# Kernel tuning notes

Measured on AMD Instinct MI355X. Metric: run time of the kernel, lower is better.

Reference implementation:

```python
import jax, jax.numpy as jnp
import numpy as np
import math

B, L, C, D, H, NLAYERS, DFF = 256, 100, 55, 512, 8, 3, 64


def _pos_embedding(length, d_model):
    pos = np.arange(length, dtype=np.float32)[:, None]
    div = np.exp(np.arange(0, d_model, 2, dtype=np.float32) * (-math.log(10000.0) / d_model))
    pe = np.zeros((length, d_model), dtype=np.float32)
    pe[:, 0::2] = np.sin(pos * div)
    pe[:, 1::2] = np.cos(pos * div)
    return jnp.asarray(pe)


def setup_inputs() -> dict:
    key = jax.random.key(0)
    ks = jax.random.split(key, 12)
    r = lambda k, s, sc: jax.random.normal(k, s, dtype=jnp.float32) * sc
    sD = 1.0 / math.sqrt(D)
    return {
        'x': r(ks[0], (B, L, C), 1.0),
        'tok_w': r(ks[1], (D, C, 3), 1.0 / math.sqrt(3 * C)),  # Conv1d(c_in->d_model, k=3, circular, no bias)
        'pe': _pos_embedding(L, D),
        'Wq': r(ks[2], (NLAYERS, D, D), sD), 'bq': jnp.zeros((NLAYERS, D), jnp.float32),
        'Wk': r(ks[3], (NLAYERS, D, D), sD), 'bk': jnp.zeros((NLAYERS, D), jnp.float32),
        'Wv': r(ks[4], (NLAYERS, D, D), sD), 'bv': jnp.zeros((NLAYERS, D), jnp.float32),
        'Wsig': r(ks[5], (NLAYERS, H, D), sD), 'bsig': jnp.zeros((NLAYERS, H), jnp.float32),
        'Wo': r(ks[6], (NLAYERS, D, D), sD), 'bo': jnp.zeros((NLAYERS, D), jnp.float32),
        'W1': r(ks[7], (NLAYERS, DFF, D), sD), 'b1': jnp.zeros((NLAYERS, DFF), jnp.float32),  # conv1 (1x1)
        'W2': r(ks[8], (NLAYERS, D, DFF), 1.0 / math.sqrt(DFF)), 'b2': jnp.zeros((NLAYERS, D), jnp.float32),  # conv2 (1x1)
        'proj_w': r(ks[9], (C, D), sD), 'proj_b': jnp.zeros((C,), jnp.float32),
    }


def _forward(x, tok_w, pe, Wq, bq, Wk, bk, Wv, bv, Wsig, bsig, Wo, bo, W1, b1, W2, b2, proj_w, proj_b):
    Bx, Lx, _ = x.shape
    nlayers, nH = Wsig.shape[0], Wsig.shape[1]
    d_model = Wq.shape[1]
    dk = d_model // nH
    scale = 1.0 / math.sqrt(dk)
    # token embedding: circular-padded Conv1d(k=3, no bias), then + positional embedding
    xc = jnp.pad(jnp.swapaxes(x, 1, 2), ((0, 0), (0, 0), (1, 1)), mode='wrap')  # [B,C,L+2]
    emb = jax.lax.conv_general_dilated(xc, tok_w, (1,), 'VALID', dimension_numbers=('NCW', 'OIW', 'NCW'))
    h = jnp.swapaxes(emb, 1, 2) + pe[None]  # [B,L,D]
    dist = jnp.abs(jnp.arange(Lx)[:, None] - jnp.arange(Lx)[None, :]).astype(h.dtype)  # |i-j|
    for l in range(nlayers):
        q = h @ Wq[l].T + bq[l]                       # [B,L,D]
        k = (h @ Wk[l].T + bk[l]).reshape(Bx, Lx, nH, dk)
        v = (h @ Wv[l].T + bv[l]).reshape(Bx, Lx, nH, dk)
        # NOTE: source applies sigma projection to the *projected* queries
        sigma = q @ Wsig[l].T + bsig[l]               # [B,L,H]
        qh = q.reshape(Bx, Lx, nH, dk)
        scores = jnp.einsum('blhe,bshe->bhls', qh, k)  # [B,H,L,L]
        series = jax.nn.softmax(scale * scores, axis=-1)
        # Gaussian prior branch (mask_flag=False; computed in source forward,
        # does not feed the module's returned output)
        sg = jnp.swapaxes(sigma, 1, 2)                 # [B,H,L]
        sg = jnp.power(3.0, jax.nn.sigmoid(sg * 5.0) + 1e-5) - 1.0
        sgE = sg[..., None]                            # [B,H,L,1]
        _prior = jnp.exp(-(dist ** 2)[None, None] / (2.0 * sgE ** 2)) / (math.sqrt(2.0 * math.pi) * sgE)
        o = jnp.einsum('bhls,bshd->blhd', series, v).reshape(Bx, Lx, d_model)
        h = h + (o @ Wo[l].T + bo[l])                  # residual 1 (dropout=identity at eval)
        y = jax.nn.gelu(h @ W1[l].T + b1[l], approximate=False)  # conv1 1x1 + gelu
        h = h + (y @ W2[l].T + b2[l])                  # conv2 1x1, residual 2
    return h @ proj_w.T + proj_b                       # [B,L,c_out]


def reference(x, tok_w, pe, Wq, bq, Wk, bk, Wv, bv, Wsig, bsig, Wo, bo, W1, b1, W2, b2, proj_w, proj_b):
    return _forward(x, tok_w, pe, Wq, bq, Wk, bk, Wv, bv, Wsig, bsig, Wo, bo, W1, b1, W2, b2, proj_w, proj_b)
```

## Files before the change

### kernel.cpp

```cpp
#include <hip/hip_runtime.h>
#include <stdint.h>

typedef unsigned short u16;
typedef __attribute__((ext_vector_type(8))) short short8;
typedef __attribute__((ext_vector_type(4))) float f32x4;

#define DEVI __device__ __forceinline__

#define BB   256
#define LL   100
#define CC   55
#define DD   512
#define HH   8
#define DKK  64
#define MM   (BB * LL)
#define KEMB 192
#define NSEG 17

DEVI float bf2f(u16 s) { union { unsigned int u; float f; } x; x.u = ((unsigned int)s) << 16; return x.f; }
DEVI u16 f2bf(float f) {
  union { float f; unsigned int u; } x; x.f = f;
  unsigned int u = x.u;
  return (u16)((u + 0x7FFFu + ((u >> 16) & 1u)) >> 16);
}

DEVI void async_lds16(const u16* gp, u16* lp) {
  __builtin_amdgcn_global_load_lds((const __attribute__((address_space(1))) void*)gp,
                                   (__attribute__((address_space(3))) void*)lp, 16, 0, 0);
}

DEVI void wave_lds_fence() {
  asm volatile("s_waitcnt lgkmcnt(0)" ::: "memory");
  __builtin_amdgcn_wave_barrier();
}

DEVI int swz_row(int r) { return (r & 3) ^ ((r >> 2) & 3); }

__global__ void detect_dtype(const u16* __restrict__ x, int* __restrict__ flag) {
  __shared__ int cnt[256];
  int tid = threadIdx.x;
  u16 u = x[2 * tid];
  int e = (u >> 7) & 0xFF;
  cnt[tid] = (e >= 0x5F && e <= 0x90) ? 1 : 0;
  __syncthreads();
  for (int s = 128; s > 0; s >>= 1) { if (tid < s) cnt[tid] += cnt[tid + s]; __syncthreads(); }
  if (tid == 0) *flag = (cnt[0] >= 160) ? 0 : 1;
}

struct Segs { const void* src[NSEG]; int off[NSEG + 1]; };

__global__ void convert_all(Segs s, const int* __restrict__ flag, u16* __restrict__ dst) {
  int i = blockIdx.x * 256 + threadIdx.x;
  if (i >= s.off[NSEG]) return;
  int sidx = 0;
#pragma unroll
  for (int k = 1; k < NSEG; k++) if (i >= s.off[k]) sidx = k;
  int j = i - s.off[sidx];
  u16 v;
  if (*flag) v = f2bf(((const float*)s.src[sidx])[j]);
  else       v = ((const u16*)s.src[sidx])[j];
  dst[i] = v;
}

__global__ void repack_w(const u16* __restrict__ tokw, u16* __restrict__ Wg) {
  int idx = blockIdx.x * 256 + threadIdx.x;
  if (idx >= 512 * KEMB) return;
  int d = idx / KEMB, j = idx % KEMB, k = j >> 6, c = j & 63;
  Wg[idx] = (c < CC) ? tokw[d * (CC * 3) + c * 3 + k] : (u16)0;
}

__global__ void repack_x(const u16* __restrict__ x, u16* __restrict__ Xg) {
  int idx = blockIdx.x * 256 + threadIdx.x;
  if (idx >= MM * KEMB) return;
  int m = idx / KEMB, j = idx % KEMB, k = j >> 6, c = j & 63;
  int b = m / LL, l = m % LL;
  int l2 = l + k - 1; l2 = (l2 + LL) % LL;
  Xg[idx] = (c < CC) ? x[(size_t)(b * LL + l2) * CC + c] : (u16)0;
}

struct GemmW { const u16* W[3]; const u16* bias[3]; void* out[3]; };

template<int BM, int BN, int NTT, int TAG, bool QKV, bool DIRECT>
__global__ __launch_bounds__(256)
void gemm_bt(const u16* __restrict__ A, int K, GemmW w,
             const u16* __restrict__ pe,
             const u16* __restrict__ resid,
             int dogelu,
             int ldo, int nvalid,
             const int* __restrict__ dtf)
{
  constexpr int BK = 32;
  constexpr int MI = BM / 32;
  constexpr int CW = BN / 2, NT = CW / 16;
  constexpr int SW = CW + 4;
  constexpr int S_BUF = (BM + BN) * BK;
  __shared__ alignas(16) u16 smem[2 * S_BUF];

  const int tid = threadIdx.x;
  const int lane = tid & 63;
  const int wv = __builtin_amdgcn_readfirstlane(tid >> 6);
  const int wm = wv & 1, wn = wv >> 1;
  const int l15 = lane & 15, qd = lane >> 4;
  const int swz = swz_row(l15);

  const int id = blockIdx.x;
  const int mpx = gridDim.x / (NTT * 8);
  const int xcd = id & 7, slot = id >> 3;
  const int m_t = xcd * mpx + slot / NTT;
  const int n_t = slot % NTT;
  const int m0 = m_t * BM;
  int n0 = n_t * BN;
  int sel = 0, n0l = n0;
  if (QKV) { sel = n0 >> 9; n0l = n0 & 511; }
  const u16* W = w.W[sel];
  const u16* bias = w.bias[sel];
  void* outp = w.out[sel];

  const f32x4 zf = {0.f, 0.f, 0.f, 0.f};
  f32x4 acc[MI][NT];
#pragma unroll
  for (int i = 0; i < MI; i++)
#pragma unroll
    for (int j = 0; j < NT; j++) acc[i][j] = zf;

  auto STAGE = [&](int buf, int kp) {
    u16* Asp = smem + buf * S_BUF;
    u16* Bsp = Asp + BM * BK;
#pragma unroll
    for (int i = 0; i < BM / 64; i++) {
      int base = i * 256 + wv * 64;
      int idx = base + lane;
      int row = idx >> 2;
      int cs = ((idx & 3) ^ swz_row(row)) * 8;
      async_lds16(A + (size_t)(m0 + row) * K + kp + cs, Asp + base * 8);
    }
#pragma unroll
    for (int i = 0; i < BN / 64; i++) {
      int base = i * 256 + wv * 64;
      int idx = base + lane;
      int row = idx >> 2;
      int cs = ((idx & 3) ^ swz_row(row)) * 8;
      int gr = n0l + row; if (gr >= nvalid) gr = nvalid - 1;
      async_lds16(W + (size_t)gr * K + kp + cs, Bsp + base * 8);
    }
  };

  const int NBK = K >> 5;
  STAGE(0, 0);
  __syncthreads();
  int cur = 0;
  for (int ks = 0; ks < NBK; ks++) {
    if (ks + 1 < NBK) STAGE(cur ^ 1, (ks + 1) << 5);
    const u16* Asp = smem + cur * S_BUF;
    const u16* Bsp = Asp + BM * BK;
    short8 af[MI], bfr[NT];
#pragma unroll
    for (int mi = 0; mi < MI; mi++)
      af[mi] = *(const short8*)&Asp[(wm * (BM / 2) + mi * 16 + l15) * BK + ((qd ^ swz) * 8)];
#pragma unroll
    for (int ni = 0; ni < NT; ni++)
      bfr[ni] = *(const short8*)&Bsp[(wn * CW + ni * 16 + l15) * BK + ((qd ^ swz) * 8)];
#pragma unroll
    for (int mi = 0; mi < MI; mi++)
#pragma unroll
      for (int ni = 0; ni < NT; ni++)
        acc[mi][ni] = __builtin_amdgcn_mfma_f32_16x16x32_bf16(af[mi], bfr[ni], acc[mi][ni], 0, 0, 0);
    __syncthreads();
    cur ^= 1;
  }

  if (DIRECT) {
    const int sf = (dtf != nullptr) ? *dtf : 0;
#pragma unroll
    for (int mi = 0; mi < MI; mi++)
#pragma unroll
      for (int ni = 0; ni < NT; ni++) {
        int gcol = n0l + wn * CW + ni * 16 + l15;
        float bv = (bias && gcol < nvalid) ? bf2f(bias[gcol]) : 0.f;
#pragma unroll
        for (int r = 0; r < 4; r++) {
          int grow = m0 + wm * (BM / 2) + mi * 16 + qd * 4 + r;
          if (gcol < nvalid) {
            float v = acc[mi][ni][r] + bv;
            if (sf) ((float*)outp)[(size_t)grow * ldo + gcol] = v;
            else    ((u16*)outp)[(size_t)grow * ldo + gcol] = f2bf(v);
          }
        }
      }
    return;
  }

  u16* slab = smem + wv * 16 * SW;
#pragma unroll
  for (int mi = 0; mi < MI; mi++) {
    const int lr = wm * (BM / 2) + mi * 16 + qd * 4;
    float v[NT][4];
    if (!QKV && resid) {
#pragma unroll
      for (int ni = 0; ni < NT; ni++) {
        int col = n0l + wn * CW + ni * 16 + l15;
#pragma unroll
        for (int r = 0; r < 4; r++)
          v[ni][r] = bf2f(resid[(size_t)(m0 + lr + r) * DD + col]);
      }
    } else {
#pragma unroll
      for (int ni = 0; ni < NT; ni++)
#pragma unroll
        for (int r = 0; r < 4; r++) v[ni][r] = 0.f;
    }
#pragma unroll
    for (int ni = 0; ni < NT; ni++) {
      const int lc = wn * CW + ni * 16 + l15;
      float bv = bias ? bf2f(bias[n0l + lc]) : 0.f;
#pragma unroll
      for (int r = 0; r < 4; r++) {
        float x = v[ni][r] + acc[mi][ni][r] + bv;
        if (!QKV && pe) x += bf2f(pe[((m0 + lr + r) % LL) * DD + n0l + lc]);
        if (!QKV && dogelu) x = 0.5f * x * (1.f + erff(x * 0.70710678118654752f));
        v[ni][r] = x;
      }
    }
#pragma unroll
    for (int ni = 0; ni < NT; ni++)
#pragma unroll
      for (int r = 0; r < 4; r++)
        slab[(qd * 4 + r) * SW + ni * 16 + l15] = f2bf(v[ni][r]);
    wave_lds_fence();
    if (BN == 128) {
      int r2 = lane >> 2, c2 = (lane & 3) * 16;
      int grow = m0 + wm * (BM / 2) + mi * 16 + r2;
      u16* op = (u16*)outp + (size_t)grow * ldo + n0l + wn * CW + c2;
      *(short8*)&op[0] = *(const short8*)&slab[r2 * SW + c2];
      *(short8*)&op[8] = *(const short8*)&slab[r2 * SW + c2 + 8];
    } else {
      if (lane < 32) {
        int r2 = lane >> 1, c2 = (lane & 1) * 16;
        int grow = m0 + wm * (BM / 2) + mi * 16 + r2;
        u16* op = (u16*)outp + (size_t)grow * ldo + n0l + wn * CW + c2;
        *(short8*)&op[0] = *(const short8*)&slab[r2 * SW + c2];
        *(short8*)&op[8] = *(const short8*)&slab[r2 * SW + c2 + 8];
      }
    }
    wave_lds_fence();
  }
}

__global__ __launch_bounds__(256)
void ffn_fused(const u16* __restrict__ h, const u16* __restrict__ W1,
               const u16* __restrict__ b1, const u16* __restrict__ W2,
               const u16* __restrict__ b2, u16* __restrict__ hout)
{
  constexpr int BM = 64, BK = 32, SW = 36;
  __shared__ alignas(16) u16 smem[4096 + 10496];
  u16* y      = smem;
  u16* shared = smem + 4096;
  u16* As  = shared;
  u16* Bs  = shared + 4096;
  u16* Bs2 = shared;
  u16* slabs = shared + 8192;

  const int tid = threadIdx.x;
  const int lane = tid & 63;
  const int wv = __builtin_amdgcn_readfirstlane(tid >> 6);
  const int wm = wv & 1, wn = wv >> 1;
  const int l15 = lane & 15, qd = lane >> 4;
  const int swz = swz_row(l15);
  const int id = blockIdx.x;
  const int mpx = gridDim.x >> 3;
  const int m0 = ((id & 7) * mpx + (id >> 3)) * BM;

  const int srow = tid >> 2;
  const int scs = ((tid & 3) ^ swz_row(srow)) * 8;
  const f32x4 zf = {0.f, 0.f, 0.f, 0.f};

  f32x4 acc[2][2];
#pragma unroll
  for (int i = 0; i < 2; i++)
#pragma unroll
    for (int j = 0; j < 2; j++) acc[i][j] = zf;

  for (int k0 = 0; k0 < DD; k0 += 64) {
    __syncthreads();
#pragma unroll
    for (int p = 0; p < 2; p++) {
      const int kp = k0 + p * BK;
      async_lds16(h  + (size_t)(m0 + srow) * DD + kp + scs, As + p * 2048 + tid * 8);
      async_lds16(W1 + (size_t)srow * DD + kp + scs,        Bs + p * 2048 + tid * 8);
    }
    __syncthreads();
#pragma unroll
    for (int p = 0; p < 2; p++) {
      short8 af[2], bfr[2];
#pragma unroll
      for (int mi = 0; mi < 2; mi++)
        af[mi] = *(const short8*)&As[p * 2048 + (wm * 32 + mi * 16 + l15) * BK + ((qd ^ swz) * 8)];
#pragma unroll
      for (int ni = 0; ni < 2; ni++)
        bfr[ni] = *(const short8*)&Bs[p * 2048 + (wn * 32 + ni * 16 + l15) * BK + ((qd ^ swz) * 8)];
#pragma unroll
      for (int mi = 0; mi < 2; mi++)
#pragma unroll
        for (int ni = 0; ni < 2; ni++)
          acc[mi][ni] = __builtin_amdgcn_mfma_f32_16x16x32_bf16(af[mi], bfr[ni], acc[mi][ni], 0, 0, 0);
    }
  }
#pragma unroll
  for (int mi = 0; mi < 2; mi++)
#pragma unroll
    for (int ni = 0; ni < 2; ni++) {
      float bv = bf2f(b1[wn * 32 + ni * 16 + l15]);
#pragma unroll
      for (int r = 0; r < 4; r++) {
        int row = wm * 32 + mi * 16 + qd * 4 + r;
        int kpos = ni * 16 + l15;
        int slot = ((kpos >> 3) ^ swz_row(row)) & 3;
        float x = acc[mi][ni][r] + bv;
        x = 0.5f * x * (1.f + erff(x * 0.70710678118654752f));
        y[wn * 2048 + row * BK + slot * 8 + (kpos & 7)] = f2bf(x);
      }
    }
  __syncthreads();

  auto stage2 = [&](int buf, int nc) {
#pragma unroll
    for (int p = 0; p < 2; p++)
      async_lds16(W2 + (size_t)(nc * 64 + srow) * 64 + p * BK + scs,
                  Bs2 + buf * 4096 + p * 2048 + tid * 8);
  };
  stage2(0, 0);
  int cur = 0;
  u16* slab = slabs + wv * 16 * SW;
  for (int nc = 0; nc < 8; nc++) {
    __syncthreads();
    if (nc + 1 < 8) stage2(cur ^ 1, nc + 1);
    f32x4 a2[2][2];
#pragma unroll
    for (int i = 0; i < 2; i++)
#pragma unroll
      for (int j = 0; j < 2; j++) a2[i][j] = zf;
#pragma unroll
    for (int p = 0; p < 2; p++) {
      short8 af[2], bfr[2];
#pragma unroll
      for (int mi = 0; mi < 2; mi++)
        af[mi] = *(const short8*)&y[p * 2048 + (wm * 32 + mi * 16 + l15) * BK + ((qd ^ swz) * 8)];
#pragma unroll
      for (int ni = 0; ni < 2; ni++)
        bfr[ni] = *(const short8*)&Bs2[cur * 4096 + p * 2048 + (wn * 32 + ni * 16 + l15) * BK + ((qd ^ swz) * 8)];
#pragma unroll
      for (int mi = 0; mi < 2; mi++)
#pragma unroll
        for (int ni = 0; ni < 2; ni++)
          a2[mi][ni] = __builtin_amdgcn_mfma_f32_16x16x32_bf16(af[mi], bfr[ni], a2[mi][ni], 0, 0, 0);
    }
    const int n0l = nc * 64;
#pragma unroll
    for (int mi = 0; mi < 2; mi++) {
      const int lr = wm * 32 + mi * 16 + qd * 4;
      float v[2][4];
#pragma unroll
      for (int ni = 0; ni < 2; ni++) {
        int col = n0l + wn * 32 + ni * 16 + l15;
        float bv = bf2f(b2[col]);
#pragma unroll
        for (int r = 0; r < 4; r++)
          v[ni][r] = bf2f(h[(size_t)(m0 + lr + r) * DD + col]) + a2[mi][ni][r] + bv;
      }
#pragma unroll
      for (int ni = 0; ni < 2; ni++)
#pragma unroll
        for (int r = 0; r < 4; r++)
          slab[(qd * 4 + r) * SW + ni * 16 + l15] = f2bf(v[ni][r]);
      wave_lds_fence();
      if (lane < 32) {
        int r2 = lane >> 1, c2 = (lane & 1) * 16;
        int grow = m0 + wm * 32 + mi * 16 + r2;
        u16* op = hout + (size_t)grow * DD + n0l + wn * 32 + c2;
        *(short8*)&op[0] = *(const short8*)&slab[r2 * SW + c2];
        *(short8*)&op[8] = *(const short8*)&slab[r2 * SW + c2 + 8];
      }
      wave_lds_fence();
    }
    cur ^= 1;
  }
}

__global__ __launch_bounds__(256)
void attn(const u16* __restrict__ qg, const u16* __restrict__ kg,
          const u16* __restrict__ vg, u16* __restrict__ og)
{
  constexpr int LP = 128;
  __shared__ alignas(16) u16 Ks[LP * DKK];
  __shared__ alignas(16) u16 Vt[DKK * LP];
  __shared__ alignas(16) u16 Ps[LP * LP];

  const int bh = blockIdx.x;
  const int b = bh >> 3, h = bh & 7;
  const size_t base = (size_t)b * LL * DD + (size_t)h * DKK;
  const int tid = threadIdx.x, lane = tid & 63, wv = tid >> 6;
  const int l15 = lane & 15, qd = lane >> 4;
  const short8 z8 = {0, 0, 0, 0, 0, 0, 0, 0};

  for (int i = tid; i < LP * 8; i += 256) {
    int row = i >> 3, e8 = (i & 7) * 8;
    short8 val = z8;
    if (row < LL) val = *(const short8*)(kg + base + (size_t)row * DD + e8);
    *(short8*)&Ks[row * DKK + e8] = val;
  }
  for (int i = tid; i < LP * 8; i += 256) {
    int j = i & 127, d0 = (i >> 7) * 8;
    short8 val = z8;
    if (j < LL) val = *(const short8*)(vg + base + (size_t)j * DD + d0);
#pragma unroll
    for (int u = 0; u < 8; u++) Vt[(d0 + u) * LP + j] = (u16)val[u];
  }
  __syncthreads();

  const f32x4 zf = {0.f, 0.f, 0.f, 0.f};
  f32x4 sc[2][8];
#pragma unroll
  for (int it = 0; it < 2; it++)
#pragma unroll
    for (int jt = 0; jt < 8; jt++) sc[it][jt] = zf;

  short8 af[2][2];
#pragma unroll
  for (int it = 0; it < 2; it++) {
    int row = (2 * wv + it) * 16 + l15;
#pragma unroll
    for (int ks = 0; ks < 2; ks++) {
      short8 val = z8;
      if (row < LL) val = *(const short8*)(qg + base + (size_t)row * DD + ks * 32 + qd * 8);
      af[it][ks] = val;
    }
  }
#pragma unroll
  for (int jt = 0; jt < 8; jt++) {
    short8 b0 = *(const short8*)&Ks[(jt * 16 + l15) * DKK + qd * 8];
    short8 b1 = *(const short8*)&Ks[(jt * 16 + l15) * DKK + 32 + qd * 8];
#pragma unroll
    for (int it = 0; it < 2; it++) {
      sc[it][jt] = __builtin_amdgcn_mfma_f32_16x16x32_bf16(af[it][0], b0, sc[it][jt], 0, 0, 0);
      sc[it][jt] = __builtin_amdgcn_mfma_f32_16x16x32_bf16(af[it][1], b1, sc[it][jt], 0, 0, 0);
    }
  }

  constexpr float scale = 0.125f;
#pragma unroll
  for (int it = 0; it < 2; it++) {
    int rb = (2 * wv + it) * 16 + qd * 4;
#pragma unroll
    for (int r = 0; r < 4; r++) {
      float vals[8];
      float mx = -1e30f;
#pragma unroll
      for (int jt = 0; jt < 8; jt++) {
        int col = jt * 16 + l15;
        float vv = sc[it][jt][r] * scale;
        if (col >= LL) vv = -1e30f;
        vals[jt] = vv;
        mx = fmaxf(mx, vv);
      }
#pragma unroll
      for (int off = 1; off < 16; off <<= 1) mx = fmaxf(mx, __shfl_xor(mx, off, 64));
      float s = 0.f;
#pragma unroll
      for (int jt = 0; jt < 8; jt++) { float p = __expf(vals[jt] - mx); vals[jt] = p; s += p; }
#pragma unroll
      for (int off = 1; off < 16; off <<= 1) s += __shfl_xor(s, off, 64);
      float inv = 1.f / s;
      int rowp = rb + r;
#pragma unroll
      for (int jt = 0; jt < 8; jt++) Ps[rowp * LP + jt * 16 + l15] = f2bf(vals[jt] * inv);
    }
  }
  __syncthreads();

  f32x4 oc[2][4];
#pragma unroll
  for (int it = 0; it < 2; it++)
#pragma unroll
    for (int dt = 0; dt < 4; dt++) oc[it][dt] = zf;
#pragma unroll
  for (int ks = 0; ks < 4; ks++) {
    short8 ap[2];
#pragma unroll
    for (int it = 0; it < 2; it++)
      ap[it] = *(const short8*)&Ps[((2 * wv + it) * 16 + l15) * LP + ks * 32 + qd * 8];
#pragma unroll
    for (int dt = 0; dt < 4; dt++) {
      short8 bv = *(const short8*)&Vt[(dt * 16 + l15) * LP + ks * 32 + qd * 8];
#pragma unroll
      for (int it = 0; it < 2; it++)
        oc[it][dt] = __builtin_amdgcn_mfma_f32_16x16x32_bf16(ap[it], bv, oc[it][dt], 0, 0, 0);
    }
  }

  __syncthreads();
  u16* Os = Ps;
#pragma unroll
  for (int it = 0; it < 2; it++) {
    int rb = (2 * wv + it) * 16 + qd * 4;
#pragma unroll
    for (int dt = 0; dt < 4; dt++)
#pragma unroll
      for (int r = 0; r < 4; r++)
        Os[(rb + r) * DKK + dt * 16 + l15] = f2bf(oc[it][dt][r]);
  }
  __syncthreads();
  {
    int row = tid >> 1, c0 = (tid & 1) * 32;
    if (row < LL) {
      u16* op = og + base + (size_t)row * DD + c0;
#pragma unroll
      for (int c = 0; c < 32; c += 8)
        *(short8*)&op[c] = *(const short8*)&Os[row * DKK + c0 + c];
    }
  }
}

extern "C" void kernel_launch(void* const* d_in, const int* in_sizes, int n_in,
                              void* d_out, int out_size, void* d_ws, size_t ws_size,
                              hipStream_t stream)
{
  (void)in_sizes; (void)n_in; (void)out_size; (void)ws_size;

  char* ws = (char*)d_ws;
  size_t off = 0;
  auto alloc = [&](size_t bytes) { char* p = ws + off; off += (bytes + 255) & ~(size_t)255; return p; };
  int* dflag = (int*)alloc(256);
  static const int seg_sizes[NSEG] = {
    MM * CC, DD * CC * 3, LL * DD,
    3 * DD * DD, 3 * DD, 3 * DD * DD, 3 * DD, 3 * DD * DD, 3 * DD,
    3 * DD * DD, 3 * DD, 3 * 64 * DD, 3 * 64, 3 * DD * 64, 3 * DD,
    CC * DD, CC
  };
  static const int seg_input[NSEG] = {0, 1, 2, 3, 4, 5, 6, 7, 8, 11, 12, 13, 14, 15, 16, 17, 18};
  int total = 0, segoff[NSEG + 1];
  for (int i = 0; i < NSEG; i++) { segoff[i] = total; total += seg_sizes[i]; }
  segoff[NSEG] = total;
  u16* canon = (u16*)alloc((size_t)total * 2);

  u16* hbf = (u16*)alloc((size_t)MM * DD * 2);
  u16* qb  = (u16*)alloc((size_t)MM * DD * 2);
  u16* kb  = (u16*)alloc((size_t)MM * DD * 2);
  u16* vb  = (u16*)alloc((size_t)MM * DD * 2);
  u16* ob  = (u16*)alloc((size_t)MM * DD * 2);
  u16* Wg  = (u16*)alloc((size_t)512 * KEMB * 2);
  u16* Xg  = qb;

  const u16* xc  = canon + segoff[0];
  const u16* twc = canon + segoff[1];
  const u16* pec = canon + segoff[2];
  const u16* Wqc = canon + segoff[3];  const u16* bqc = canon + segoff[4];
  const u16* Wkc = canon + segoff[5];  const u16* bkc = canon + segoff[6];
  const u16* Wvc = canon + segoff[7];  const u16* bvc = canon + segoff[8];
  const u16* Woc = canon + segoff[9];  const u16* boc = canon + segoff[10];
  const u16* W1c = canon + segoff[11]; const u16* b1c = canon + segoff[12];
  const u16* W2c = canon + segoff[13]; const u16* b2c = canon + segoff[14];
  const u16* pwc = canon + segoff[15]; const u16* pbc = canon + segoff[16];

  Segs sg;
  for (int i = 0; i < NSEG; i++) { sg.src[i] = d_in[seg_input[i]]; sg.off[i] = segoff[i]; }
  sg.off[NSEG] = total;

  dim3 blk(256);
  detect_dtype<<<dim3(1), blk, 0, stream>>>((const u16*)d_in[0], dflag);
  convert_all<<<dim3((total + 255) / 256), blk, 0, stream>>>(sg, dflag, canon);
  repack_w<<<dim3((512 * KEMB + 255) / 256), blk, 0, stream>>>(twc, Wg);
  repack_x<<<dim3((MM * KEMB + 255) / 256), blk, 0, stream>>>(xc, Xg);

  auto W1of = [&](const u16* p) { GemmW g{}; g.W[0] = g.W[1] = g.W[2] = p; return g; };

  { GemmW g = W1of(Wg); g.out[0] = hbf;
    gemm_bt<128, 64, 8, 0, false, false><<<dim3(1600), blk, 0, stream>>>(Xg, KEMB, g, pec, nullptr, 0, DD, DD, nullptr); }

  for (int l = 0; l < 3; l++) {
    const u16* Wq_l = Wqc + (size_t)l * DD * DD; const u16* bq_l = bqc + l * DD;
    const u16* Wk_l = Wkc + (size_t)l * DD * DD; const u16* bk_l = bkc + l * DD;
    const u16* Wv_l = Wvc + (size_t)l * DD * DD; const u16* bv_l = bvc + l * DD;
    const u16* Wo_l = Woc + (size_t)l * DD * DD; const u16* bo_l = boc + l * DD;
    const u16* W1_l = W1c + (size_t)l * 64 * DD; const u16* b1_l = b1c + l * 64;
    const u16* W2_l = W2c + (size_t)l * DD * 64; const u16* b2_l = b2c + l * DD;

    { GemmW g{}; g.W[0] = Wq_l; g.W[1] = Wk_l; g.W[2] = Wv_l;
      g.bias[0] = bq_l; g.bias[1] = bk_l; g.bias[2] = bv_l;
      g.out[0] = qb; g.out[1] = kb; g.out[2] = vb;
      gemm_bt<128, 64, 24, 1, true, false><<<dim3(4800), blk, 0, stream>>>(hbf, DD, g, nullptr, nullptr, 0, DD, DD, nullptr); }

    attn<<<dim3(BB * HH), blk, 0, stream>>>(qb, kb, vb, ob);

    { GemmW g = W1of(Wo_l); g.bias[0] = g.bias[1] = g.bias[2] = bo_l; g.out[0] = g.out[1] = g.out[2] = hbf;
      gemm_bt<128, 64, 8, 2, false, false><<<dim3(1600), blk, 0, stream>>>(ob, DD, g, nullptr, hbf, 0, DD, DD, nullptr); }

    ffn_fused<<<dim3(400), blk, 0, stream>>>(hbf, W1_l, b1_l, W2_l, b2_l, hbf);
  }
  { GemmW g = W1of(pwc); g.bias[0] = pbc; g.out[0] = d_out;
    gemm_bt<64, 64, 1, 5, false, true><<<dim3(400), blk, 0, stream>>>(hbf, DD, g, nullptr, nullptr, 0, CC, CC, dflag); }
}
```

Before: 682.0 us.

## Triple-buffer GEMM K-loop with vmcnt-based waits instead of full syncthreads

Moves the bt GEMM main loop from double to triple buffering in LDS, issuing async global-to-LDS loads two stages ahead. Each iteration waits only on the older loads via explicit s_waitcnt vmcnt and a bare s_barrier, rather than a __syncthreads after every compute step. This aims to hide global load latency and cut barrier stalls. The cost is 1.5x the shared memory, which may lower occupancy, plus fragile hand-counted vmcnt values that depend on how many loads each stage issues.

New measurement: 668.6 us. -2.0%, faster.

```diff
diff --git a/kernel.cpp b/kernel.cpp
--- a/kernel.cpp
+++ b/kernel.cpp
@@ -94,7 +94,8 @@
   constexpr int CW = BN / 2, NT = CW / 16;
   constexpr int SW = CW + 4;
   constexpr int S_BUF = (BM + BN) * BK;
-  __shared__ alignas(16) u16 smem[2 * S_BUF];
+  constexpr int VPS = BM / 64 + BN / 64;
+  __shared__ alignas(16) u16 smem[3 * S_BUF];
 
   const int tid = threadIdx.x;
   const int lane = tid & 63;
@@ -145,29 +146,53 @@
     }
   };
 
+  auto COMPUTE = [&](int buf) {
+    const u16* Asp = smem + buf * S_BUF;
+    const u16* Bsp = Asp + BM * BK;
+    short8 af[MI], bfr[NT];
+#pragma unroll
+    for (int mi = 0; mi < MI; mi++)
+      af[mi] = *(const short8*)&Asp[(wm * (BM / 2) + mi * 16 + l15) * BK + ((qd ^ swz) * 8)];
+#pragma unroll
+    for (int ni = 0; ni < NT; ni++)
+      bfr[ni] = *(const short8*)&Bsp[(wn * CW + ni * 16 + l15) * BK + ((qd ^ swz) * 8)];
+#pragma unroll
+    for (int mi = 0; mi < MI; mi++)
+#pragma unroll
+      for (int ni = 0; ni < NT; ni++)
+        acc[mi][ni] = __builtin_amdgcn_mfma_f32_16x16x32_bf16(af[mi], bfr[ni], acc[mi][ni], 0, 0, 0);
+  };
+
+  auto WAITV = [] {
+    if constexpr (VPS == 2)      asm volatile("s_waitcnt vmcnt(2)" ::: "memory");
+    else if constexpr (VPS == 3) asm volatile("s_waitcnt vmcnt(3)" ::: "memory");
+    else                         asm volatile("s_waitcnt vmcnt(4)" ::: "memory");
+  };
+
   const int NBK = K >> 5;
   STAGE(0, 0);
-  __syncthreads();
-  int cur = 0;
-  for (int ks = 0; ks < NBK; ks++) {
-    if (ks + 1 < NBK) STAGE(cur ^ 1, (ks + 1) << 5);
-    const u16* Asp = smem + cur * S_BUF;
-    const u16* Bsp = Asp + BM * BK;
-    short8 af[MI], bfr[NT];
-#pragma unroll
-    for (int mi = 0; mi < MI; mi++)
-      af[mi] = *(const short8*)&Asp[(wm * (BM / 2) + mi * 16 + l15) * BK + ((qd ^ swz) * 8)];
-#pragma unroll
-    for (int ni = 0; ni < NT; ni++)
-      bfr[ni] = *(const short8*)&Bsp[(wn * CW + ni * 16 + l15) * BK + ((qd ^ swz) * 8)];
-#pragma unroll
-    for (int mi = 0; mi < MI; mi++)
-#pragma unroll
-      for (int ni = 0; ni < NT; ni++)
-        acc[mi][ni] = __builtin_amdgcn_mfma_f32_16x16x32_bf16(af[mi], bfr[ni], acc[mi][ni], 0, 0, 0);
-    __syncthreads();
-    cur ^= 1;
-  }
+  STAGE(1, BK);
+  int cur = 0, st = 2;
+  for (int ks = 0; ks < NBK - 2; ks++) {
+    WAITV();
+    __builtin_amdgcn_s_barrier();
+    asm volatile("" ::: "memory");
+    STAGE(st, (ks + 2) << 5);
+    COMPUTE(cur);
+    asm volatile("s_waitcnt lgkmcnt(0)" ::: "memory");
+    cur = (cur == 2) ? 0 : cur + 1;
+    st  = (st  == 2) ? 0 : st  + 1;
+  }
+  WAITV();
+  __builtin_amdgcn_s_barrier();
+  asm volatile("" ::: "memory");
+  COMPUTE(cur);
+  asm volatile("s_waitcnt lgkmcnt(0)" ::: "memory");
+  cur = (cur == 2) ? 0 : cur + 1;
+  asm volatile("s_waitcnt vmcnt(0)" ::: "memory");
+  __builtin_amdgcn_s_barrier();
+  asm volatile("" ::: "memory");
+  COMPUTE(cur);
 
   if (DIRECT) {
     const int sf = (dtf != nullptr) ? *dtf : 0;
@@ -190,6 +215,7 @@
     return;
   }
 
+  __syncthreads();
   u16* slab = smem + wv * 16 * SW;
 #pragma unroll
   for (int mi = 0; mi < MI; mi++) {
```
